# Kernel optimization log

Hardware: AMD Instinct MI355X
Metric: run time of the kernel (lower is better)

Reference implementation:

```python
import jax, jax.numpy as jnp
import numpy as np

B, S, D, H, K = 2, 1024, 1024, 16, 33  # batch, seq, d_model, heads, rel buckets (k+1)
d = D // H


def setup_inputs() -> dict:
    key = jax.random.key(0)
    ks = jax.random.split(key, 16)
    w = lambda k, shape: jax.random.normal(k, shape, dtype=jnp.float32) * 0.02
    return {
        "hidden_state": jax.random.normal(ks[0], (B, S, D), dtype=jnp.float32),
        "pos_indices": jax.random.randint(ks[1], (B, S, S), 0, K),
        "mask": jax.random.bernoulli(ks[2], 0.1, (B, 1, 1, S)),
        "Wq": w(ks[3], (D, D)), "bq": w(ks[4], (D,)),
        "Wk": w(ks[5], (D, D)), "bk": w(ks[6], (D,)),
        "Wv": w(ks[7], (D, D)), "bv": w(ks[8], (D,)),
        "Wo": w(ks[9], (D, D)), "bo": w(ks[10], (D,)),
        "rel_q": w(ks[11], (H, K, d)),
        "rel_k": w(ks[12], (H, K, d)),
        "rel_v": w(ks[13], (H, K, d)),
    }


def reference(hidden_state, pos_indices, mask, Wq, bq, Wk, bk, Wv, bv, Wo, bo,
              rel_q, rel_k, rel_v):
    b, s, dm = hidden_state.shape
    h, k_, dp = rel_q.shape
    # projections -> [B,H,S,d]
    def proj(x, W, bias):
        return (x @ W + bias).reshape(b, s, h, dp).transpose(0, 2, 1, 3)
    q = proj(hidden_state, Wq, bq)
    kk = proj(hidden_state, Wk, bk)
    v = proj(hidden_state, Wv, bv)
    # scale_factor = 1 (c2c) + 1 (rel_q) + 1 (rel_k)
    scale = 1.0 / np.sqrt(dp * 3).astype(np.float32)
    # content-to-content
    c2c = jnp.einsum("bhid,bhjd->bhij", q, kk) * scale
    idx = jnp.broadcast_to(pos_indices[:, None], (b, h, s, s))
    # position-to-content: raw [B,H,K,S], gathered along K with per-(i,j) bucket
    raw_p2c = jnp.einsum("hkd,bhjd->bhkj", rel_q, kk) * scale
    p2c = jnp.take_along_axis(raw_p2c, idx, axis=2)
    # content-to-position: raw [B,H,S,K], gathered along K
    raw_c2p = jnp.einsum("bhid,hkd->bhik", q, rel_k) * scale
    c2p = jnp.take_along_axis(raw_c2p, idx, axis=3)
    scores = c2c + p2c + c2p
    scores = jnp.where(mask, jnp.float32(-1e9), scores)
    probs = jax.nn.softmax(scores, axis=-1)  # dropout is identity in eval
    ctx = jnp.einsum("bhij,bhjd->bhid", probs, v)
    # value-side relative term: sum_j P[i,j] * rel_v[bucket(i,j)]
    oh = jax.nn.one_hot(pos_indices, k_, dtype=probs.dtype)  # [B,S,S,K]
    agg = jnp.einsum("bhij,bijk->bhik", probs, oh)
    ctx = ctx + jnp.einsum("bhik,hkd->bhid", agg, rel_v)
    out = ctx.transpose(0, 2, 1, 3).reshape(b, s, dm)
    return out @ Wo + bo
```

## Files before the change

### kernel.cpp

```cpp
#include <hip/hip_runtime.h>
#include <hip/hip_bf16.h>

#define B_ 2
#define S_ 1024
#define D_ 1024
#define H_ 16
#define K_ 33
#define DH 64
#define SCALE 0.07216878364870322f
#define LOG2E 1.4426950408889634f
#define SCALEL (SCALE * LOG2E)
#define FXS 32768.0f
#define FXI (1.0f / 32768.0f)

typedef __attribute__((ext_vector_type(8))) short bf16x8;
typedef __attribute__((ext_vector_type(4))) float f32x4;

__device__ __forceinline__ float b2f(unsigned short u) {
    return __uint_as_float(((unsigned int)u) << 16);
}
__device__ __forceinline__ unsigned short f2b(float f) {
    unsigned int u = __float_as_uint(f);
    u += 0x7FFFu + ((u >> 16) & 1u);
    return (unsigned short)(u >> 16);
}
__device__ __forceinline__ float ldf(const void* p, int i, int f32) {
    return f32 ? ((const float*)p)[i] : b2f(((const unsigned short*)p)[i]);
}
__device__ __forceinline__ float4 ldf4(const void* p, int i, int f32) {
    if (f32) return *(const float4*)((const float*)p + i);
    ushort4 u = *(const ushort4*)((const unsigned short*)p + i);
    return make_float4(b2f(u.x), b2f(u.y), b2f(u.z), b2f(u.w));
}
__device__ __forceinline__ float4 ldb4(const unsigned short* p, int i) {
    ushort4 u = *(const ushort4*)(p + i);
    return make_float4(b2f(u.x), b2f(u.y), b2f(u.z), b2f(u.w));
}
__device__ __forceinline__ int sniff_f32(const void* hidden) {
    __shared__ int cnt;
    if (threadIdx.x == 0) cnt = 0;
    __syncthreads();
    const unsigned short* hu = (const unsigned short*)hidden;
    int c = 0;
    for (int i = threadIdx.x; i < 2048; i += 256) {
        int e = (hu[i] >> 7) & 0xFF;
        if (e >= 0x8E) c++;
    }
    if (c) atomicAdd(&cnt, c);
    __syncthreads();
    return (cnt >= 8) ? 1 : 0;
}

__global__ __launch_bounds__(256) void setup_fused(const void* __restrict__ hidden,
                                                   const void* __restrict__ mask,
                                                   const int* __restrict__ pos,
                                                   const void* __restrict__ W0,
                                                   const void* __restrict__ W1,
                                                   const void* __restrict__ W2,
                                                   const void* __restrict__ W3,
                                                   int* __restrict__ flags,
                                                   float* __restrict__ mflag,
                                                   unsigned char* __restrict__ pos8,
                                                   unsigned short* __restrict__ T0,
                                                   unsigned short* __restrict__ T1,
                                                   unsigned short* __restrict__ T2,
                                                   unsigned short* __restrict__ T3) {
    const int bid = blockIdx.x;
    const int t = threadIdx.x;
    if (bid < 2048) {
        int i = bid * 256 + t;
        if (i < (B_ * S_ * S_) / 4) {
            int4 p = *(const int4*)&pos[i * 4];
            uchar4 o;
            o.x = (unsigned char)min(max(p.x, 0), K_ - 1);
            o.y = (unsigned char)min(max(p.y, 0), K_ - 1);
            o.z = (unsigned char)min(max(p.z, 0), K_ - 1);
            o.w = (unsigned char)min(max(p.w, 0), K_ - 1);
            *(uchar4*)&pos8[i * 4] = o;
        }
        return;
    }
    if (bid < 3072) {
        const int f32u = sniff_f32(hidden);
        __shared__ unsigned short tl[64][66];
        int r = bid - 2048;
        int z = r >> 8;
        int wy = (r & 255) >> 4, wx = r & 15;
        const void* W = z == 0 ? W0 : (z == 1 ? W1 : (z == 2 ? W2 : W3));
        unsigned short* T = z == 0 ? T0 : (z == 1 ? T1 : (z == 2 ? T2 : T3));
        const int k0 = wy * 64, n0 = wx * 64;
        {
            int kr = t >> 2, nc = (t & 3) * 16;
#pragma unroll
            for (int u = 0; u < 4; ++u) {
                float4 v = ldf4(W, (k0 + kr) * 1024 + n0 + nc + u * 4, f32u);
                tl[kr][nc + u * 4 + 0] = f2b(v.x);
                tl[kr][nc + u * 4 + 1] = f2b(v.y);
                tl[kr][nc + u * 4 + 2] = f2b(v.z);
                tl[kr][nc + u * 4 + 3] = f2b(v.w);
            }
        }
        __syncthreads();
        {
            int nr = t >> 2, kc = (t & 3) * 16;
            unsigned short o[16];
#pragma unroll
            for (int u = 0; u < 16; ++u) o[u] = tl[kc + u][nr];
#pragma unroll
            for (int u = 0; u < 4; ++u)
                *(ushort4*)&T[(n0 + nr) * 1024 + k0 + kc + u * 4] = *(ushort4*)&o[u * 4];
        }
        return;
    }
    {
        __shared__ int mev[6];
        const int f32u = sniff_f32(hidden);
        if (t < 6) mev[t] = 0;
        __syncthreads();
        const unsigned char* mb = (const unsigned char*)mask;
        int e_bf = 0, e_f32 = 0, e_f64 = 0, e_f16 = 0, e_u8 = 0;
        for (int p = t; p < 2048; p += 256) {
            unsigned char v = mb[p];
            if ((p & 7) == 6 && v == 0xF0) e_f64 = 1;
            if ((p & 3) == 1 && v == 0x3F) e_bf = 1;
            if ((p & 3) == 3 && v == 0x3F) e_f32 = 1;
            if ((p & 1) == 1 && v == 0x3C) e_f16 = 1;
            if ((p & 3) != 0 && v != 0) e_u8 = 1;
        }
        if (e_f64) atomicOr(&mev[5], 1);
        if (e_bf)  atomicOr(&mev[3], 1);
        if (e_f32) atomicOr(&mev[2], 1);
        if (e_f16) atomicOr(&mev[4], 1);
        if (e_u8)  atomicOr(&mev[1], 1);
        __syncthreads();
        const int mm = mev[5] ? 5 : (mev[3] ? 3 : (mev[2] ? 2 : (mev[4] ? 4 : (mev[1] ? 1 : 0))));
        if (t == 0) { flags[0] = f32u; flags[2] = mm; }
        for (int j = t; j < B_ * S_; j += 256) {
            int m;
            if (mm == 5)      m = (((const double*)mask)[j] != 0.0);
            else if (mm == 3 || mm == 4) m = (((const unsigned short*)mask)[j] != 0);
            else if (mm == 2) m = (((const float*)mask)[j] != 0.f);
            else if (mm == 1) m = (mb[j] != 0);
            else              m = (((const int*)mask)[j] != 0);
            mflag[j] = m ? 1.f : 0.f;
        }
    }
}

__global__ __launch_bounds__(256) void prep(const void* __restrict__ hidden,
                                            const void* __restrict__ mask,
                                            int* __restrict__ flags,
                                            float* __restrict__ mflag) {
    __shared__ int mev[6];
    const int t = threadIdx.x;
    const int f32u = sniff_f32(hidden);
    if (t < 6) mev[t] = 0;
    __syncthreads();
    const unsigned char* mb = (const unsigned char*)mask;
    int e_bf = 0, e_f32 = 0, e_f64 = 0, e_f16 = 0, e_u8 = 0;
    for (int p = t; p < 2048; p += 256) {
        unsigned char v = mb[p];
        if ((p & 7) == 6 && v == 0xF0) e_f64 = 1;
        if ((p & 3) == 1 && v == 0x3F) e_bf = 1;
        if ((p & 3) == 3 && v == 0x3F) e_f32 = 1;
        if ((p & 1) == 1 && v == 0x3C) e_f16 = 1;
        if ((p & 3) != 0 && v != 0) e_u8 = 1;
    }
    if (e_f64) atomicOr(&mev[5], 1);
    if (e_bf)  atomicOr(&mev[3], 1);
    if (e_f32) atomicOr(&mev[2], 1);
    if (e_f16) atomicOr(&mev[4], 1);
    if (e_u8)  atomicOr(&mev[1], 1);
    __syncthreads();
    const int mm = mev[5] ? 5 : (mev[3] ? 3 : (mev[2] ? 2 : (mev[4] ? 4 : (mev[1] ? 1 : 0))));
    if (t == 0) { flags[0] = f32u; flags[2] = mm; }
    for (int j = t; j < B_ * S_; j += 256) {
        int m;
        if (mm == 5)      m = (((const double*)mask)[j] != 0.0);
        else if (mm == 3 || mm == 4) m = (((const unsigned short*)mask)[j] != 0);
        else if (mm == 2) m = (((const float*)mask)[j] != 0.f);
        else if (mm == 1) m = (mb[j] != 0);
        else              m = (((const int*)mask)[j] != 0);
        mflag[j] = m ? 1.f : 0.f;
    }
}

__global__ __launch_bounds__(256) void pos_pack(const int* __restrict__ pos,
                                                unsigned char* __restrict__ pos8) {
    int i = blockIdx.x * 256 + threadIdx.x;
    if (i >= (B_ * S_ * S_) / 4) return;
    int4 p = *(const int4*)&pos[i * 4];
    uchar4 o;
    o.x = (unsigned char)min(max(p.x, 0), K_ - 1);
    o.y = (unsigned char)min(max(p.y, 0), K_ - 1);
    o.z = (unsigned char)min(max(p.z, 0), K_ - 1);
    o.w = (unsigned char)min(max(p.w, 0), K_ - 1);
    *(uchar4*)&pos8[i * 4] = o;
}

__global__ __launch_bounds__(256, 3) void gemm_qkv_mfma(const void* __restrict__ X,
                                                        const void* __restrict__ W0,
                                                        const void* __restrict__ W1,
                                                        const void* __restrict__ W2,
                                                        const unsigned short* __restrict__ T0,
                                                        const unsigned short* __restrict__ T1,
                                                        const unsigned short* __restrict__ T2,
                                                        const void* __restrict__ b0,
                                                        const void* __restrict__ b1,
                                                        const void* __restrict__ b2,
                                                        const int* __restrict__ flags, int useT,
                                                        unsigned short* __restrict__ q,
                                                        unsigned short* __restrict__ kk_,
                                                        unsigned short* __restrict__ v) {
    __shared__ unsigned short Asl[128][40];
    __shared__ unsigned short Bsl[64][40];
    const int f32u = flags[0];
    const int z = blockIdx.z;
    const void* W = z == 0 ? W0 : (z == 1 ? W1 : W2);
    const unsigned short* WT = z == 0 ? T0 : (z == 1 ? T1 : T2);
    const void* bias = z == 0 ? b0 : (z == 1 ? b1 : b2);
    unsigned short* outp = z == 0 ? q : (z == 1 ? kk_ : v);
    const int m0 = blockIdx.y * 128, n0 = blockIdx.x * 64;
    const int t = threadIdx.x;
    const int w = t >> 6, lane = t & 63;
    const int wr = w >> 1, wc = w & 1;
    const int lm = lane & 15, lg = lane >> 4;

    const int am = t >> 1, ac16 = (t & 1) * 16;
    const int bn = t >> 2, bk8 = (t & 3) * 8;
    const int fbn = t & 63, fbkq = (t >> 6) * 8;

    f32x4 acc[4][2] = {};
    float4 pa[4];
    ushort4 tb0, tb1;
    float pbx[8];

    {
        int base = (m0 + am) * 1024 + ac16;
#pragma unroll
        for (int u = 0; u < 4; ++u) pa[u] = ldf4(X, base + u * 4, f32u);
        if (useT) {
            const ushort4* s = (const ushort4*)&WT[(n0 + bn) * 1024 + bk8];
            tb0 = s[0]; tb1 = s[1];
        } else {
#pragma unroll
            for (int qi = 0; qi < 8; ++qi)
                pbx[qi] = ldf(W, (fbkq + qi) * 1024 + n0 + fbn, f32u);
        }
    }

    for (int k0 = 0; k0 < 1024; k0 += 32) {
        {
#pragma unroll
            for (int u = 0; u < 4; ++u) {
                ushort4 uv = {f2b(pa[u].x), f2b(pa[u].y), f2b(pa[u].z), f2b(pa[u].w)};
                *(ushort4*)&Asl[am][ac16 + u * 4] = uv;
            }
            if (useT) {
                *(ushort4*)&Bsl[bn][bk8] = tb0;
                *(ushort4*)&Bsl[bn][bk8 + 4] = tb1;
            } else {
#pragma unroll
                for (int qi = 0; qi < 8; qi += 2) {
                    unsigned int pk = (unsigned int)f2b(pbx[qi]) |
                                      ((unsigned int)f2b(pbx[qi + 1]) << 16);
                    *(unsigned int*)&Bsl[fbn][fbkq + qi] = pk;
                }
            }
        }
        __syncthreads();
        if (k0 + 32 < 1024) {
            int kn = k0 + 32;
            int base = (m0 + am) * 1024 + kn + ac16;
#pragma unroll
            for (int u = 0; u < 4; ++u) pa[u] = ldf4(X, base + u * 4, f32u);
            if (useT) {
                const ushort4* s = (const ushort4*)&WT[(n0 + bn) * 1024 + kn + bk8];
                tb0 = s[0]; tb1 = s[1];
            } else {
#pragma unroll
                for (int qi = 0; qi < 8; ++qi)
                    pbx[qi] = ldf(W, (kn + fbkq + qi) * 1024 + n0 + fbn, f32u);
            }
        }
        bf16x8 af[4], bfr[2];
#pragma unroll
        for (int mi = 0; mi < 4; ++mi)
            af[mi] = *(const bf16x8*)&Asl[wr * 64 + mi * 16 + lm][lg * 8];
#pragma unroll
        for (int nj = 0; nj < 2; ++nj)
            bfr[nj] = *(const bf16x8*)&Bsl[wc * 32 + nj * 16 + lm][lg * 8];
#pragma unroll
        for (int mi = 0; mi < 4; ++mi)
#pragma unroll
            for (int nj = 0; nj < 2; ++nj)
                acc[mi][nj] = __builtin_amdgcn_mfma_f32_16x16x32_bf16(af[mi], bfr[nj],
                                                                      acc[mi][nj], 0, 0, 0);
        __syncthreads();
    }
#pragma unroll
    for (int nj = 0; nj < 2; ++nj) {
        int n = n0 + wc * 32 + nj * 16 + lm;
        float bv = ldf(bias, n, f32u);
        int hh = n >> 6, dd = n & 63;
#pragma unroll
        for (int mi = 0; mi < 4; ++mi) {
#pragma unroll
            for (int r = 0; r < 4; ++r) {
                int m = m0 + wr * 64 + mi * 16 + lg * 4 + r;
                int bb = m >> 10, ii = m & 1023;
                outp[((bb * H_ + hh) * S_ + ii) * DH + dd] = f2b(acc[mi][nj][r] + bv);
            }
        }
    }
}

__global__ __launch_bounds__(256, 3) void gemm_out_mfma(const unsigned short* __restrict__ X,
                                                        const void* __restrict__ W,
                                                        const unsigned short* __restrict__ WT,
                                                        const void* __restrict__ bias,
                                                        const int* __restrict__ flags, int useT,
                                                        float* __restrict__ out) {
    __shared__ unsigned short Asl[128][40];
    __shared__ unsigned short Bsl[64][40];
    const int f32u = flags[0];
    const int m0 = blockIdx.y * 128, n0 = blockIdx.x * 64;
    const int t = threadIdx.x;
    const int w = t >> 6, lane = t & 63;
    const int wr = w >> 1, wc = w & 1;
    const int lm = lane & 15, lg = lane >> 4;

    const int am = t >> 1, ac16 = (t & 1) * 16;
    const int bn = t >> 2, bk8 = (t & 3) * 8;
    const int fbn = t & 63, fbkq = (t >> 6) * 8;

    f32x4 acc[4][2] = {};
    ushort4 pa[4];
    ushort4 tb0, tb1;
    float pbx[8];

    {
        const ushort4* src = (const ushort4*)&X[(m0 + am) * 1024 + ac16];
#pragma unroll
        for (int u = 0; u < 4; ++u) pa[u] = src[u];
        if (useT) {
            const ushort4* s = (const ushort4*)&WT[(n0 + bn) * 1024 + bk8];
            tb0 = s[0]; tb1 = s[1];
        } else {
#pragma unroll
            for (int qi = 0; qi < 8; ++qi)
                pbx[qi] = ldf(W, (fbkq + qi) * 1024 + n0 + fbn, f32u);
        }
    }

    for (int k0 = 0; k0 < 1024; k0 += 32) {
        {
#pragma unroll
            for (int u = 0; u < 4; ++u) *(ushort4*)&Asl[am][ac16 + u * 4] = pa[u];
            if (useT) {
                *(ushort4*)&Bsl[bn][bk8] = tb0;
                *(ushort4*)&Bsl[bn][bk8 + 4] = tb1;
            } else {
#pragma unroll
                for (int qi = 0; qi < 8; qi += 2) {
                    unsigned int pk = (unsigned int)f2b(pbx[qi]) |
                                      ((unsigned int)f2b(pbx[qi + 1]) << 16);
                    *(unsigned int*)&Bsl[fbn][fbkq + qi] = pk;
                }
            }
        }
        __syncthreads();
        if (k0 + 32 < 1024) {
            int kn = k0 + 32;
            const ushort4* src = (const ushort4*)&X[(m0 + am) * 1024 + kn + ac16];
#pragma unroll
            for (int u = 0; u < 4; ++u) pa[u] = src[u];
            if (useT) {
                const ushort4* s = (const ushort4*)&WT[(n0 + bn) * 1024 + kn + bk8];
                tb0 = s[0]; tb1 = s[1];
            } else {
#pragma unroll
                for (int qi = 0; qi < 8; ++qi)
                    pbx[qi] = ldf(W, (kn + fbkq + qi) * 1024 + n0 + fbn, f32u);
            }
        }
        bf16x8 af[4], bfr[2];
#pragma unroll
        for (int mi = 0; mi < 4; ++mi)
            af[mi] = *(const bf16x8*)&Asl[wr * 64 + mi * 16 + lm][lg * 8];
#pragma unroll
        for (int nj = 0; nj < 2; ++nj)
            bfr[nj] = *(const bf16x8*)&Bsl[wc * 32 + nj * 16 + lm][lg * 8];
#pragma unroll
        for (int mi = 0; mi < 4; ++mi)
#pragma unroll
            for (int nj = 0; nj < 2; ++nj)
                acc[mi][nj] = __builtin_amdgcn_mfma_f32_16x16x32_bf16(af[mi], bfr[nj],
                                                                      acc[mi][nj], 0, 0, 0);
        __syncthreads();
    }
#pragma unroll
    for (int nj = 0; nj < 2; ++nj) {
        int n = n0 + wc * 32 + nj * 16 + lm;
        float bv = ldf(bias, n, f32u);
#pragma unroll
        for (int mi = 0; mi < 4; ++mi) {
#pragma unroll
            for (int r = 0; r < 4; ++r) {
                int m = m0 + wr * 64 + mi * 16 + lg * 4 + r;
                out[m * 1024 + n] = acc[mi][nj][r] + bv;
            }
        }
    }
}

__global__ __launch_bounds__(256) void rel_fused(const unsigned short* __restrict__ kws,
                                                 const unsigned short* __restrict__ qws,
                                                 const void* __restrict__ relq,
                                                 const void* __restrict__ relk,
                                                 const int* __restrict__ flags,
                                                 unsigned short* __restrict__ p2c,
                                                 unsigned short* __restrict__ c2p) {
    __shared__ float xt[64][68];
    __shared__ float rr[33][68];
    const int f32u = flags[0];
    const int bh = blockIdx.y, h = bh & 15;
    const int x0 = blockIdx.x * 64;
    const int t = threadIdx.x;
    if (blockIdx.z == 0) {
#pragma unroll
        for (int qq = 0; qq < 4; ++qq) {
            int idx = t + 256 * qq;
            int j = idx >> 4, d4 = idx & 15;
            *(float4*)&xt[j][d4 * 4] = ldb4(kws, (bh * S_ + x0 + j) * DH + d4 * 4);
        }
        for (int idx = t; idx < 33 * 16; idx += 256) {
            int k = idx >> 4, d4 = idx & 15;
            *(float4*)&rr[k][d4 * 4] = ldf4(relq, (h * K_ + k) * DH + d4 * 4, f32u);
        }
        __syncthreads();
        for (int o = t; o < 33 * 64; o += 256) {
            int k = o >> 6, j = o & 63;
            float s = 0.f;
#pragma unroll
            for (int d4 = 0; d4 < 16; ++d4) {
                float4 a = *(const float4*)&rr[k][d4 * 4];
                float4 b = *(const float4*)&xt[j][d4 * 4];
                s += a.x * b.x + a.y * b.y + a.z * b.z + a.w * b.w;
            }
            p2c[(bh * K_ + k) * S_ + x0 + j] = f2b(s * SCALEL);
        }
    } else {
#pragma unroll
        for (int qq = 0; qq < 4; ++qq) {
            int idx = t + 256 * qq;
            int i = idx >> 4, d4 = idx & 15;
            *(float4*)&xt[i][d4 * 4] = ldb4(qws, (bh * S_ + x0 + i) * DH + d4 * 4);
        }
        for (int idx = t; idx < 33 * 16; idx += 256) {
            int k = idx >> 4, d4 = idx & 15;
            *(float4*)&rr[k][d4 * 4] = ldf4(relk, (h * K_ + k) * DH + d4 * 4, f32u);
        }
        __syncthreads();
        for (int o = t; o < 64 * 33; o += 256) {
            int i = o / 33, k = o % 33;
            float s = 0.f;
#pragma unroll
            for (int d4 = 0; d4 < 16; ++d4) {
                float4 a = *(const float4*)&xt[i][d4 * 4];
                float4 b = *(const float4*)&rr[k][d4 * 4];
                s += a.x * b.x + a.y * b.y + a.z * b.z + a.w * b.w;
            }
            c2p[(bh * S_ + x0 + i) * K_ + k] = f2b(s * SCALEL);
        }
    }
}

#define PS_OFF   0
#define VT_OFF   16384
#define P2CS_OFF 16384
#define C2P_OFF  33792
#define AG_OFF   38144
#define RV_OFF   46848
#define MF_OFF   51072
#define ATTN_LDS 52096

__device__ __forceinline__ int ps_addr(int il, int jc) {
    return PS_OFF + il * 256 +
           ((jc * 2) ^ ((((il >> 2) & 3) << 5) ^ ((il & 3) << 4)));
}

__global__ __launch_bounds__(512, 4) void attn_mfma(const unsigned short* __restrict__ qws,
                                                    const unsigned short* __restrict__ kws,
                                                    const unsigned short* __restrict__ vws,
                                                    const unsigned short* __restrict__ p2c,
                                                    const unsigned short* __restrict__ c2p,
                                                    const float* __restrict__ mflag,
                                                    const unsigned char* __restrict__ pos8,
                                                    const int* __restrict__ pos32,
                                                    int use8,
                                                    const void* __restrict__ relv,
                                                    const int* __restrict__ flags,
                                                    unsigned short* __restrict__ ctxo) {
    extern __shared__ char smem[];
    const int f32u = flags[0];
    const int lin = blockIdx.y * 16 + blockIdx.x;
    const int logi = (lin & 7) * 64 + (lin >> 3);
    const int bh = logi >> 4, b = bh >> 4, h = bh & 15;
    const int i0 = (logi & 15) * 64;
    const int t = threadIdx.x;
    const int w = t >> 6, lane = t & 63;
    const int lm = lane & 15, lg = lane >> 4;
    const int iband = (w & 3) * 16;
    const int jh = w >> 2;
    const int dbase = jh * 32;

    unsigned int* agU = (unsigned int*)(smem + AG_OFF);
    unsigned short* c2pS = (unsigned short*)(smem + C2P_OFF);
    unsigned short* rvS = (unsigned short*)(smem + RV_OFF);
    unsigned char* mfS = (unsigned char*)(smem + MF_OFF);

    for (int idx = t; idx < 64 * 33; idx += 512) {
        int il = idx / 33, k = idx % 33;
        c2pS[il * 34 + k] = c2p[(bh * S_ + i0 + il) * K_ + k];
    }
    for (int idx = t; idx < 33 * 64; idx += 512) {
        int k = idx >> 6, d = idx & 63;
        rvS[k * 64 + d] = f2b(ldf(relv, (h * K_ + k) * DH + d, f32u));
    }
    for (int idx = t; idx < 1024; idx += 512)
        mfS[idx] = (mflag[b * S_ + idx] != 0.f) ? 1 : 0;
    for (int idx = t; idx < 64 * 34; idx += 512) agU[idx] = 0u;

    bf16x8 aq0 = *(const bf16x8*)&qws[(bh * S_ + i0 + iband + lm) * DH + lg * 8];
    bf16x8 aq1 = *(const bf16x8*)&qws[(bh * S_ + i0 + iband + lm) * DH + 32 + lg * 8];
    f32x4 acc0 = {}, acc1 = {};

    const int p2cbase = bh * K_ * S_;
    const int rowbase = (b * S_ + i0 + iband + lg * 4) * S_;
    __syncthreads();

    for (int c = 0; c < 8; ++c) {
        for (int idx = t; idx < 33 * 16; idx += 512) {
            int k = idx >> 4, v8 = idx & 15;
            uint4 src = *(const uint4*)&p2c[p2cbase + k * S_ + c * 128 + v8 * 8];
            unsigned int* dst = (unsigned int*)(smem + P2CS_OFF + k * 260 + v8 * 16);
            dst[0] = src.x; dst[1] = src.y; dst[2] = src.z; dst[3] = src.w;
        }
        __syncthreads();

        for (int jt = 0; jt < 4; ++jt) {
            const int jc = jh * 64 + jt * 16 + lm;
            const int jcol = c * 128 + jc;
            int pb4[4];
            if (use8) {
#pragma unroll
                for (int r = 0; r < 4; ++r)
                    pb4[r] = pos8[rowbase + r * S_ + jcol];
            } else {
#pragma unroll
                for (int r = 0; r < 4; ++r) {
                    int p = pos32[rowbase + r * S_ + jcol];
                    pb4[r] = min(max(p, 0), K_ - 1);
                }
            }
            bf16x8 kf0 = *(const bf16x8*)&kws[(bh * S_ + jcol) * DH + lg * 8];
            bf16x8 kf1 = *(const bf16x8*)&kws[(bh * S_ + jcol) * DH + 32 + lg * 8];
            f32x4 a = {};
            a = __builtin_amdgcn_mfma_f32_16x16x32_bf16(aq0, kf0, a, 0, 0, 0);
            a = __builtin_amdgcn_mfma_f32_16x16x32_bf16(aq1, kf1, a, 0, 0, 0);
            const int masked = mfS[jcol];
#pragma unroll
            for (int r = 0; r < 4; ++r) {
                int il = iband + lg * 4 + r;
                int pb = pb4[r];
                float gv = b2f(*(const unsigned short*)(smem + P2CS_OFF + pb * 260 + jc * 2));
                float s = a[r] * SCALEL + gv + b2f(c2pS[il * 34 + pb]);
                float ev = masked ? 0.f : exp2f(s);
                *(unsigned short*)(smem + ps_addr(il, jc)) = f2b(ev);
                atomicAdd(&agU[il * 34 + pb], (unsigned int)(ev * FXS));
            }
        }
        __syncthreads();

#pragma unroll
        for (int u = 0; u < 2; ++u) {
            int idx = t + u * 512;
            int jj = idx >> 3;
            int a8 = idx & 7;
            int d0 = a8 * 8;
            int j = c * 128 + jj;
            bf16x8 vv = *(const bf16x8*)&vws[(bh * S_ + j) * DH + d0];
#pragma unroll
            for (int e = 0; e < 8; ++e) {
                int ee = (e + a8) & 7;
                *(unsigned short*)(smem + VT_OFF + (d0 + ee) * 272 + jj * 2) =
                    ((short*)&vv)[ee];
            }
        }
        __syncthreads();

#pragma unroll
        for (int ks = 0; ks < 4; ++ks) {
            int jcb = ks * 32 + lg * 8;
            bf16x8 af = *(const bf16x8*)(smem + ps_addr(iband + lm, jcb));
            bf16x8 b0 = *(const bf16x8*)(smem + VT_OFF + (dbase + lm) * 272 +
                                         (ks * 32 + lg * 8) * 2);
            bf16x8 b1 = *(const bf16x8*)(smem + VT_OFF + (dbase + 16 + lm) * 272 +
                                         (ks * 32 + lg * 8) * 2);
            acc0 = __builtin_amdgcn_mfma_f32_16x16x32_bf16(af, b0, acc0, 0, 0, 0);
            acc1 = __builtin_amdgcn_mfma_f32_16x16x32_bf16(af, b1, acc1, 0, 0, 0);
        }
        __syncthreads();
    }

#pragma unroll
    for (int r = 0; r < 4; ++r) {
        int il = iband + lg * 4 + r;
        float rs = 0.f;
        float o0 = acc0[r], o1 = acc1[r];
        for (int kb = 0; kb < K_; ++kb) {
            float a = (float)agU[il * 34 + kb] * FXI;
            rs += a;
            o0 += a * b2f(rvS[kb * 64 + dbase + lm]);
            o1 += a * b2f(rvS[kb * 64 + dbase + 16 + lm]);
        }
        float inv = 1.0f / rs;
        ctxo[(b * S_ + i0 + il) * D_ + h * DH + dbase + lm] = f2b(o0 * inv);
        ctxo[(b * S_ + i0 + il) * D_ + h * DH + dbase + 16 + lm] = f2b(o1 * inv);
    }
}

extern "C" void kernel_launch(void* const* d_in, const int* in_sizes, int n_in,
                              void* d_out, int out_size, void* d_ws, size_t ws_size,
                              hipStream_t stream) {
    const void* hidden = d_in[0];
    const void* pos = d_in[1];
    const void* mask = d_in[2];
    const void* Wq = d_in[3];
    const void* bq = d_in[4];
    const void* Wk = d_in[5];
    const void* bk = d_in[6];
    const void* Wv = d_in[7];
    const void* bv = d_in[8];
    const void* Wo = d_in[9];
    const void* bo = d_in[10];
    const void* rq = d_in[11];
    const void* rk = d_in[12];
    const void* rv = d_in[13];

    unsigned char* wsb = (unsigned char*)d_ws;
    size_t o = 0;
    int* flags = (int*)(wsb + o);            o += 256;
    float* mfl = (float*)(wsb + o);          o += 2048 * 4;
    o = (o + 255) & ~(size_t)255;
    unsigned short* qb   = (unsigned short*)(wsb + o); o += 4194304;
    unsigned short* kb   = (unsigned short*)(wsb + o); o += 4194304;
    unsigned short* vb   = (unsigned short*)(wsb + o); o += 4194304;
    unsigned short* p2cb = (unsigned short*)(wsb + o); o += 2162688;
    unsigned short* c2pb = (unsigned short*)(wsb + o); o += 2162688;
    unsigned short* ctxb = (unsigned short*)(wsb + o); o += 4194304;
    unsigned char* pos8  = (unsigned char*)(wsb + o);  o += 2097152;
    const int use8 = (ws_size >= o) ? 1 : 0;
    unsigned short* wTq = (unsigned short*)(wsb + o);  o += 2097152;
    unsigned short* wTk = (unsigned short*)(wsb + o);  o += 2097152;
    unsigned short* wTv = (unsigned short*)(wsb + o);  o += 2097152;
    unsigned short* wTo = (unsigned short*)(wsb + o);  o += 2097152;
    const int useT = (ws_size >= o) ? 1 : 0;

    float* out = (float*)d_out;
    const int* posi = (const int*)pos;

    hipFuncSetAttribute(reinterpret_cast<const void*>(attn_mfma),
                        hipFuncAttributeMaxDynamicSharedMemorySize, ATTN_LDS);

    dim3 tb(256);
    if (use8 && useT) {
        setup_fused<<<dim3(3073), tb, 0, stream>>>(hidden, mask, posi, Wq, Wk, Wv, Wo,
                                                   flags, mfl, pos8, wTq, wTk, wTv, wTo);
    } else {
        prep<<<dim3(1), tb, 0, stream>>>(hidden, mask, flags, mfl);
        if (use8) pos_pack<<<dim3(2048), tb, 0, stream>>>(posi, pos8);
    }
    gemm_qkv_mfma<<<dim3(16, 16, 3), tb, 0, stream>>>(hidden, Wq, Wk, Wv,
                                                      wTq, wTk, wTv,
                                                      bq, bk, bv, flags, useT,
                                                      qb, kb, vb);
    rel_fused<<<dim3(16, 32, 2), tb, 0, stream>>>(kb, qb, rq, rk, flags, p2cb, c2pb);
    attn_mfma<<<dim3(16, 32), dim3(512), ATTN_LDS, stream>>>(qb, kb, vb, p2cb, c2pb, mfl,
                                                             pos8, posi, use8, rv, flags,
                                                             ctxb);
    gemm_out_mfma<<<dim3(16, 16), tb, 0, stream>>>(ctxb, Wo, wTo, bo, flags, useT,
                                                   out);
}
```

Measured before the change: 151.0 us.

## Shrink attention tiles to 16 query rows and 64-key chunks with 256-thread blocks

Restructures the attention kernel so each block handles 16 query rows instead of 64, using 4 waves of 256 threads that each own a 16-column key slice and a 16-wide output slice, and processes keys in 64-column chunks. LDS drops from about 52KB to about 20KB, and the grid grows fourfold to 2048 blocks, aiming for more resident blocks per CU and better load balance. The cost is that K/V/p2c chunks are reloaded by four times as many blocks, rel_v and the mask are staged per block more often, and per-block setup and barrier overhead rises relative to compute.

Result: slower. 192.9 us (+27.7%).

```diff
diff --git a/kernel.cpp b/kernel.cpp
--- a/kernel.cpp
+++ b/kernel.cpp
@@ -477,20 +477,20 @@
 }
 
 #define PS_OFF   0
-#define VT_OFF   16384
-#define P2CS_OFF 16384
-#define C2P_OFF  33792
-#define AG_OFF   38144
-#define RV_OFF   46848
-#define MF_OFF   51072
-#define ATTN_LDS 52096
+#define VT_OFF   2048
+#define P2CS_OFF 2048
+#define C2P_OFF  11264
+#define AG_OFF   12352
+#define RV_OFF   14528
+#define MF_OFF   18752
+#define ATTN_LDS 19776
 
 __device__ __forceinline__ int ps_addr(int il, int jc) {
-    return PS_OFF + il * 256 +
+    return PS_OFF + il * 128 +
            ((jc * 2) ^ ((((il >> 2) & 3) << 5) ^ ((il & 3) << 4)));
 }
 
-__global__ __launch_bounds__(512, 4) void attn_mfma(const unsigned short* __restrict__ qws,
+__global__ __launch_bounds__(256, 6) void attn_mfma(const unsigned short* __restrict__ qws,
                                                     const unsigned short* __restrict__ kws,
                                                     const unsigned short* __restrict__ vws,
                                                     const unsigned short* __restrict__ p2c,
@@ -505,53 +505,51 @@
     extern __shared__ char smem[];
     const int f32u = flags[0];
     const int lin = blockIdx.y * 16 + blockIdx.x;
-    const int logi = (lin & 7) * 64 + (lin >> 3);
-    const int bh = logi >> 4, b = bh >> 4, h = bh & 15;
-    const int i0 = (logi & 15) * 64;
+    const int logi = (lin & 7) * 256 + (lin >> 3);
+    const int bh = logi >> 6, b = bh >> 4, h = bh & 15;
+    const int i0 = (logi & 63) * 16;
     const int t = threadIdx.x;
     const int w = t >> 6, lane = t & 63;
     const int lm = lane & 15, lg = lane >> 4;
-    const int iband = (w & 3) * 16;
-    const int jh = w >> 2;
-    const int dbase = jh * 32;
+    const int dbase = w * 16;
 
     unsigned int* agU = (unsigned int*)(smem + AG_OFF);
     unsigned short* c2pS = (unsigned short*)(smem + C2P_OFF);
     unsigned short* rvS = (unsigned short*)(smem + RV_OFF);
     unsigned char* mfS = (unsigned char*)(smem + MF_OFF);
 
-    for (int idx = t; idx < 64 * 33; idx += 512) {
+    for (int idx = t; idx < 16 * 33; idx += 256) {
         int il = idx / 33, k = idx % 33;
         c2pS[il * 34 + k] = c2p[(bh * S_ + i0 + il) * K_ + k];
     }
-    for (int idx = t; idx < 33 * 64; idx += 512) {
+    for (int idx = t; idx < 33 * 64; idx += 256) {
         int k = idx >> 6, d = idx & 63;
         rvS[k * 64 + d] = f2b(ldf(relv, (h * K_ + k) * DH + d, f32u));
     }
-    for (int idx = t; idx < 1024; idx += 512)
+    for (int idx = t; idx < 1024; idx += 256)
         mfS[idx] = (mflag[b * S_ + idx] != 0.f) ? 1 : 0;
-    for (int idx = t; idx < 64 * 34; idx += 512) agU[idx] = 0u;
-
-    bf16x8 aq0 = *(const bf16x8*)&qws[(bh * S_ + i0 + iband + lm) * DH + lg * 8];
-    bf16x8 aq1 = *(const bf16x8*)&qws[(bh * S_ + i0 + iband + lm) * DH + 32 + lg * 8];
-    f32x4 acc0 = {}, acc1 = {};
+    for (int idx = t; idx < 16 * 34; idx += 256) agU[idx] = 0u;
+
+    bf16x8 aq0 = *(const bf16x8*)&qws[(bh * S_ + i0 + lm) * DH + lg * 8];
+    bf16x8 aq1 = *(const bf16x8*)&qws[(bh * S_ + i0 + lm) * DH + 32 + lg * 8];
+    f32x4 acc0 = {};
 
     const int p2cbase = bh * K_ * S_;
-    const int rowbase = (b * S_ + i0 + iband + lg * 4) * S_;
+    const int rowbase = (b * S_ + i0 + lg * 4) * S_;
     __syncthreads();
 
-    for (int c = 0; c < 8; ++c) {
-        for (int idx = t; idx < 33 * 16; idx += 512) {
-            int k = idx >> 4, v8 = idx & 15;
-            uint4 src = *(const uint4*)&p2c[p2cbase + k * S_ + c * 128 + v8 * 8];
-            unsigned int* dst = (unsigned int*)(smem + P2CS_OFF + k * 260 + v8 * 16);
+    for (int c = 0; c < 16; ++c) {
+        for (int idx = t; idx < 33 * 8; idx += 256) {
+            int k = idx >> 3, v8 = idx & 7;
+            uint4 src = *(const uint4*)&p2c[p2cbase + k * S_ + c * 64 + v8 * 8];
+            unsigned int* dst = (unsigned int*)(smem + P2CS_OFF + k * 132 + v8 * 16);
             dst[0] = src.x; dst[1] = src.y; dst[2] = src.z; dst[3] = src.w;
         }
         __syncthreads();
 
-        for (int jt = 0; jt < 4; ++jt) {
-            const int jc = jh * 64 + jt * 16 + lm;
-            const int jcol = c * 128 + jc;
+        {
+            const int jc = w * 16 + lm;
+            const int jcol = c * 64 + jc;
             int pb4[4];
             if (use8) {
 #pragma unroll
@@ -572,9 +570,9 @@
             const int masked = mfS[jcol];
 #pragma unroll
             for (int r = 0; r < 4; ++r) {
-                int il = iband + lg * 4 + r;
+                int il = lg * 4 + r;
                 int pb = pb4[r];
-                float gv = b2f(*(const unsigned short*)(smem + P2CS_OFF + pb * 260 + jc * 2));
+                float gv = b2f(*(const unsigned short*)(smem + P2CS_OFF + pb * 132 + jc * 2));
                 float s = a[r] * SCALEL + gv + b2f(c2pS[il * 34 + pb]);
                 float ev = masked ? 0.f : exp2f(s);
                 *(unsigned short*)(smem + ps_addr(il, jc)) = f2b(ev);
@@ -585,49 +583,43 @@
 
 #pragma unroll
         for (int u = 0; u < 2; ++u) {
-            int idx = t + u * 512;
+            int idx = t + u * 256;
             int jj = idx >> 3;
             int a8 = idx & 7;
             int d0 = a8 * 8;
-            int j = c * 128 + jj;
+            int j = c * 64 + jj;
             bf16x8 vv = *(const bf16x8*)&vws[(bh * S_ + j) * DH + d0];
 #pragma unroll
             for (int e = 0; e < 8; ++e) {
                 int ee = (e + a8) & 7;
-                *(unsigned short*)(smem + VT_OFF + (d0 + ee) * 272 + jj * 2) =
+                *(unsigned short*)(smem + VT_OFF + (d0 + ee) * 144 + jj * 2) =
                     ((short*)&vv)[ee];
             }
         }
         __syncthreads();
 
 #pragma unroll
-        for (int ks = 0; ks < 4; ++ks) {
+        for (int ks = 0; ks < 2; ++ks) {
             int jcb = ks * 32 + lg * 8;
-            bf16x8 af = *(const bf16x8*)(smem + ps_addr(iband + lm, jcb));
-            bf16x8 b0 = *(const bf16x8*)(smem + VT_OFF + (dbase + lm) * 272 +
-                                         (ks * 32 + lg * 8) * 2);
-            bf16x8 b1 = *(const bf16x8*)(smem + VT_OFF + (dbase + 16 + lm) * 272 +
+            bf16x8 af = *(const bf16x8*)(smem + ps_addr(lm, jcb));
+            bf16x8 b0 = *(const bf16x8*)(smem + VT_OFF + (dbase + lm) * 144 +
                                          (ks * 32 + lg * 8) * 2);
             acc0 = __builtin_amdgcn_mfma_f32_16x16x32_bf16(af, b0, acc0, 0, 0, 0);
-            acc1 = __builtin_amdgcn_mfma_f32_16x16x32_bf16(af, b1, acc1, 0, 0, 0);
         }
         __syncthreads();
     }
 
 #pragma unroll
     for (int r = 0; r < 4; ++r) {
-        int il = iband + lg * 4 + r;
+        int il = lg * 4 + r;
         float rs = 0.f;
-        float o0 = acc0[r], o1 = acc1[r];
+        float o0 = acc0[r];
         for (int kb = 0; kb < K_; ++kb) {
             float a = (float)agU[il * 34 + kb] * FXI;
             rs += a;
             o0 += a * b2f(rvS[kb * 64 + dbase + lm]);
-            o1 += a * b2f(rvS[kb * 64 + dbase + 16 + lm]);
-        }
-        float inv = 1.0f / rs;
-        ctxo[(b * S_ + i0 + il) * D_ + h * DH + dbase + lm] = f2b(o0 * inv);
-        ctxo[(b * S_ + i0 + il) * D_ + h * DH + dbase + 16 + lm] = f2b(o1 * inv);
+        }
+        ctxo[(b * S_ + i0 + il) * D_ + h * DH + dbase + lm] = f2b(o0 / rs);
     }
 }
 
@@ -687,9 +679,9 @@
                                                       bq, bk, bv, flags, useT,
                                                       qb, kb, vb);
     rel_fused<<<dim3(16, 32, 2), tb, 0, stream>>>(kb, qb, rq, rk, flags, p2cb, c2pb);
-    attn_mfma<<<dim3(16, 32), dim3(512), ATTN_LDS, stream>>>(qb, kb, vb, p2cb, c2pb, mfl,
-                                                             pos8, posi, use8, rv, flags,
-                                                             ctxb);
+    attn_mfma<<<dim3(16, 128), tb, ATTN_LDS, stream>>>(qb, kb, vb, p2cb, c2pb, mfl,
+                                                       pos8, posi, use8, rv, flags,
+                                                       ctxb);
     gemm_out_mfma<<<dim3(16, 16), tb, 0, stream>>>(ctxb, Wo, wTo, bo, flags, useT,
                                                    out);
 }
```
